# Kernel optimization log

Measured on AMD Instinct MI355X. Metric: run time of the kernel, lower is better.

Reference implementation:

```python
import jax, jax.numpy as jnp
import numpy as np

NUM_EMBEDDINGS = 1024
EMBEDDING_DIM = 256


def setup_inputs() -> dict:
    key = jax.random.key(0)
    k1, k2 = jax.random.split(key)
    z_e = jax.random.normal(k1, (32, EMBEDDING_DIM, 32, 32), dtype=jnp.float32)
    codebook = jax.random.normal(k2, (NUM_EMBEDDINGS, EMBEDDING_DIM), dtype=jnp.float32)
    return {"z_e": z_e, "codebook": codebook}


def reference(z_e, codebook):
    # z_e: [B, C, H, W] with C == embedding_dim; codebook: [K, C]
    B, C, H, W = z_e.shape
    K = codebook.shape[0]
    # _flatten: NCHW -> NHWC -> [N, C]
    z_nhwc = jnp.transpose(z_e, (0, 2, 3, 1))
    z_flat = z_nhwc.reshape(-1, C)
    # _compute_distances: ||z||^2 + ||e||^2 - 2 z e^T  -> [N, K]
    z_sq = jnp.sum(z_flat * z_flat, axis=1, keepdims=True)
    e_sq = jnp.sum(codebook * codebook, axis=1)
    distances = z_sq + e_sq - 2.0 * jnp.matmul(z_flat, codebook.T)
    # argmin + one-hot scatter (_build_encodings)
    indices = jnp.argmin(distances, axis=1)
    encodings = jax.nn.one_hot(indices, K, dtype=z_flat.dtype)  # [N, K]
    # _compute_perplexity
    avg_probs = jnp.mean(encodings, axis=0)
    perplexity = jnp.exp(-jnp.sum(avg_probs * jnp.log(avg_probs + 1e-10)))
    return distances, indices, encodings, perplexity
```

## Files before the change

### kernel.cpp

```cpp
#include <hip/hip_runtime.h>
#include <math.h>

#define N_ROWS 32768
#define K_CODES 1024
#define C_DIM 256
#define HW 1024

#define OFF_DIST 0
#define OFF_IDX  (N_ROWS * K_CODES)
#define OFF_ENC  (OFF_IDX + N_ROWS)
#define OFF_PERP (OFF_ENC + N_ROWS * K_CODES)

typedef __attribute__((ext_vector_type(8))) short short8;
typedef __attribute__((ext_vector_type(4))) float f32x4;

__device__ inline unsigned short bf16_rn(float x) {
    unsigned int u = __float_as_uint(x);
    unsigned int r = u + 0x7FFFu + ((u >> 16) & 1u);
    return (unsigned short)(r >> 16);
}
__device__ inline float bf16_to_f(unsigned short h) {
    return __uint_as_float(((unsigned int)h) << 16);
}

__device__ __forceinline__ void gl2lds16(const unsigned short* g, char* l) {
    __builtin_amdgcn_global_load_lds(
        (const __attribute__((address_space(1))) unsigned int*)g,
        (__attribute__((address_space(3))) unsigned int*)l, 16, 0, 0);
}

__global__ __launch_bounds__(256) void prep_kernel(
        const float* __restrict__ z, const float* __restrict__ cb,
        unsigned short* __restrict__ z_hi, unsigned short* __restrict__ z_lo,
        unsigned short* __restrict__ cb_hi, unsigned short* __restrict__ cb_lo,
        float* __restrict__ zsq, float* __restrict__ esq) {
    const int bid = blockIdx.x;
    const int t = threadIdx.x;

    if (bid >= 256) {
        const int lane = t & 63;
        const int k = (bid - 256) * 4 + (t >> 6);
        float4 v = *reinterpret_cast<const float4*>(cb + (size_t)k * C_DIM + lane * 4);
        float s = v.x * v.x + v.y * v.y + v.z * v.z + v.w * v.w;
        ushort4 h, l;
        h.x = bf16_rn(v.x); l.x = bf16_rn(v.x - bf16_to_f(h.x));
        h.y = bf16_rn(v.y); l.y = bf16_rn(v.y - bf16_to_f(h.y));
        h.z = bf16_rn(v.z); l.z = bf16_rn(v.z - bf16_to_f(h.z));
        h.w = bf16_rn(v.w); l.w = bf16_rn(v.w - bf16_to_f(h.w));
        *reinterpret_cast<ushort4*>(cb_hi + (size_t)k * C_DIM + lane * 4) = h;
        *reinterpret_cast<ushort4*>(cb_lo + (size_t)k * C_DIM + lane * 4) = l;
#pragma unroll
        for (int m = 1; m < 64; m <<= 1) s += __shfl_xor(s, m);
        if (lane == 0) esq[k] = s;
        return;
    }

    __shared__ float st[64][132];
    const int b = bid >> 3;
    const int hw0 = (bid & 7) * 128;

    const int c_r  = t >> 5;
    const int hw_r = (t & 31) * 4;
    const int hw_w = t >> 1;
    const int ch   = (t & 1) * 32;
    const int n    = b * HW + hw0 + hw_w;

    float zacc = 0.f;

    for (int c0 = 0; c0 < C_DIM; c0 += 64) {
#pragma unroll
        for (int it = 0; it < 8; ++it) {
            int c_l = it * 8 + c_r;
            float4 v = *reinterpret_cast<const float4*>(
                z + (size_t)b * (C_DIM * HW) + (size_t)(c0 + c_l) * HW + hw0 + hw_r);
            *reinterpret_cast<float4*>(&st[c_l][hw_r]) = v;
        }
        __syncthreads();

        short8 hv[4], lv[4];
#pragma unroll
        for (int j = 0; j < 32; ++j) {
            float x = st[ch + j][hw_w];
            unsigned short h = bf16_rn(x);
            unsigned short lo = bf16_rn(x - bf16_to_f(h));
            hv[j >> 3][j & 7] = (short)h;
            lv[j >> 3][j & 7] = (short)lo;
            zacc = fmaf(x, x, zacc);
        }
        unsigned short* hp = z_hi + (size_t)n * C_DIM + c0 + ch;
        unsigned short* lp = z_lo + (size_t)n * C_DIM + c0 + ch;
#pragma unroll
        for (int q = 0; q < 4; ++q) {
            *reinterpret_cast<short8*>(hp + q * 8) = hv[q];
            *reinterpret_cast<short8*>(lp + q * 8) = lv[q];
        }
        __syncthreads();
    }
    float o = __shfl_xor(zacc, 1);
    if ((t & 1) == 0) zsq[n] = zacc + o;
}

#define KSTEPS 24

__global__ __launch_bounds__(512) void dist_mfma_kernel(
        const unsigned short* __restrict__ z_hi,
        const unsigned short* __restrict__ z_lo,
        const unsigned short* __restrict__ cb_hi,
        const unsigned short* __restrict__ cb_lo,
        const float* __restrict__ zsq, const float* __restrict__ esq,
        float* __restrict__ dist, float2* __restrict__ partial) {
    __shared__ __align__(16) unsigned short As[2][128 * 32];
    __shared__ __align__(16) unsigned short Bs[2][256 * 32];
    __shared__ float2 pb[128][4];

    const int t = threadIdx.x;
    const int lane = t & 63, wid = t >> 6;
    const int wy = wid >> 2, wx = wid & 3;
    const int l15 = lane & 15, l4 = lane >> 4;

    const int swz = (blockIdx.x & 7) * 128 + (blockIdx.x >> 3);
    const int kbi = swz & 3;
    const int kb = kbi * 256;
    const int nb = (swz >> 2) * 128;

#define STAGE(buf_, s_) do {                                                   \
        const int sp_ = (s_) >> 3;                                             \
        const int sc0_ = ((s_) & 7) * 32;                                      \
        const unsigned short* Ap_ = (sp_ == 2) ? z_lo : z_hi;                  \
        const unsigned short* Bp_ = (sp_ == 1) ? cb_lo : cb_hi;                \
        const int wb_ = (t & ~63) * 16;                                        \
        gl2lds16(Ap_ + (size_t)(nb + (t >> 2)) * C_DIM + sc0_ + (t & 3) * 8,   \
                 (char*)(&As[buf_][0]) + wb_);                                 \
        gl2lds16(Bp_ + (size_t)(kb + (t >> 2)) * C_DIM + sc0_ + (t & 3) * 8,   \
                 (char*)(&Bs[buf_][0]) + wb_);                                 \
        gl2lds16(Bp_ + (size_t)(kb + 128 + (t >> 2)) * C_DIM + sc0_ + (t & 3) * 8, \
                 (char*)(&Bs[buf_][0]) + 8192 + wb_);                          \
    } while (0)

    f32x4 acc[4][4] = {};

    STAGE(0, 0);
    __syncthreads();

    for (int s = 0; s < KSTEPS; ++s) {
        const int cur = s & 1;
        if (s < KSTEPS - 1) STAGE(cur ^ 1, s + 1);

        short8 av[4], bv[4];
#pragma unroll
        for (int mi = 0; mi < 4; ++mi)
            av[mi] = *reinterpret_cast<const short8*>(
                &As[cur][(wy * 64 + mi * 16 + l15) * 32 + l4 * 8]);
#pragma unroll
        for (int ci = 0; ci < 4; ++ci)
            bv[ci] = *reinterpret_cast<const short8*>(
                &Bs[cur][(wx * 64 + ci * 16 + l15) * 32 + l4 * 8]);

#pragma unroll
        for (int mi = 0; mi < 4; ++mi)
#pragma unroll
            for (int ci = 0; ci < 4; ++ci)
                acc[mi][ci] = __builtin_amdgcn_mfma_f32_16x16x32_bf16(
                    av[mi], bv[ci], acc[mi][ci], 0, 0, 0);
        __syncthreads();
    }
#undef STAGE

    float zsv[4][4];
#pragma unroll
    for (int mi = 0; mi < 4; ++mi)
#pragma unroll
        for (int r = 0; r < 4; ++r)
            zsv[mi][r] = zsq[nb + wy * 64 + mi * 16 + l4 * 4 + r];
    float esv[4];
#pragma unroll
    for (int ci = 0; ci < 4; ++ci)
        esv[ci] = esq[kb + wx * 64 + ci * 16 + l15];

    float best[4][4];
    int bidx[4][4];
#pragma unroll
    for (int mi = 0; mi < 4; ++mi)
#pragma unroll
        for (int r = 0; r < 4; ++r) { best[mi][r] = 1e30f; bidx[mi][r] = K_CODES; }

#pragma unroll
    for (int mi = 0; mi < 4; ++mi) {
#pragma unroll
        for (int r = 0; r < 4; ++r) {
            int row = nb + wy * 64 + mi * 16 + l4 * 4 + r;
            float* drow = dist + (size_t)row * K_CODES;
#pragma unroll
            for (int ci = 0; ci < 4; ++ci) {
                int col = kb + wx * 64 + ci * 16 + l15;
                float d = zsv[mi][r] + esv[ci] - 2.f * acc[mi][ci][r];
                drow[col] = d;
                if (d < best[mi][r]) { best[mi][r] = d; bidx[mi][r] = col; }
            }
        }
    }

#pragma unroll
    for (int m = 1; m < 16; m <<= 1) {
#pragma unroll
        for (int mi = 0; mi < 4; ++mi)
#pragma unroll
            for (int r = 0; r < 4; ++r) {
                float ob = __shfl_xor(best[mi][r], m);
                int   oi = __shfl_xor(bidx[mi][r], m);
                if (ob < best[mi][r] || (ob == best[mi][r] && oi < bidx[mi][r])) {
                    best[mi][r] = ob; bidx[mi][r] = oi;
                }
            }
    }

    if (l15 == 0) {
#pragma unroll
        for (int mi = 0; mi < 4; ++mi)
#pragma unroll
            for (int r = 0; r < 4; ++r) {
                int rl = wy * 64 + mi * 16 + l4 * 4 + r;
                pb[rl][wx] = make_float2(best[mi][r], (float)bidx[mi][r]);
            }
    }
    __syncthreads();
    if (t < 128) {
        float2 bv2 = pb[t][0];
#pragma unroll
        for (int w = 1; w < 4; ++w) {
            float2 c = pb[t][w];
            if (c.x < bv2.x) bv2 = c;
        }
        partial[(size_t)kbi * N_ROWS + nb + t] = bv2;
    }
}

__global__ __launch_bounds__(256) void combenc_kernel(
        const float2* __restrict__ partial, float* __restrict__ idx_out,
        int* __restrict__ idx_int, float* __restrict__ enc) {
    __shared__ int sidx[16];
    const int t = threadIdx.x;
    const int r0 = blockIdx.x * 16;
    if (t < 16) {
        int n = r0 + t;
        float2 bv = partial[n];
#pragma unroll
        for (int kb = 1; kb < 4; ++kb) {
            float2 c = partial[(size_t)kb * N_ROWS + n];
            if (c.x < bv.x) bv = c;
        }
        idx_out[n] = bv.y;
        idx_int[n] = (int)bv.y;
        sidx[t] = (int)bv.y;
    }
    __syncthreads();
    const int k0 = t * 4;
#pragma unroll 4
    for (int r = 0; r < 16; ++r) {
        int bi = sidx[r];
        float4 v;
        v.x = (k0 + 0 == bi) ? 1.0f : 0.0f;
        v.y = (k0 + 1 == bi) ? 1.0f : 0.0f;
        v.z = (k0 + 2 == bi) ? 1.0f : 0.0f;
        v.w = (k0 + 3 == bi) ? 1.0f : 0.0f;
        *reinterpret_cast<float4*>(enc + (size_t)(r0 + r) * K_CODES + k0) = v;
    }
}

__global__ __launch_bounds__(1024) void perp_kernel(const int* __restrict__ idxi,
                                                    float* __restrict__ out) {
    __shared__ int hist[K_CODES];
    __shared__ float wsum[16];
    const int t = threadIdx.x;
    hist[t] = 0;
    __syncthreads();
    for (int n = t; n < N_ROWS; n += 1024)
        atomicAdd(&hist[idxi[n]], 1);
    __syncthreads();
    float p = (float)hist[t] * (1.0f / (float)N_ROWS);
    float s = p * logf(p + 1e-10f);
#pragma unroll
    for (int off = 32; off > 0; off >>= 1) s += __shfl_down(s, off);
    if ((t & 63) == 0) wsum[t >> 6] = s;
    __syncthreads();
    if (t == 0) {
        float tot = 0.f;
#pragma unroll
        for (int w = 0; w < 16; ++w) tot += wsum[w];
        out[0] = expf(-tot);
    }
}

extern "C" void kernel_launch(void* const* d_in, const int* in_sizes, int n_in,
                              void* d_out, int out_size, void* d_ws, size_t ws_size,
                              hipStream_t stream) {
    const float* z  = (const float*)d_in[0];
    const float* cb = (const float*)d_in[1];
    float* out  = (float*)d_out;
    float* dist = out + OFF_DIST;
    float* idxo = out + OFF_IDX;
    float* enc  = out + OFF_ENC;
    float* perp = out + OFF_PERP;

    char* wsb = (char*)d_ws;
    float*  zsq  = (float*)(wsb + 0);
    float*  esq  = (float*)(wsb + 131072);
    int*    idxi = (int*)(wsb + 135168);
    float2* part = (float2*)(wsb + 266240);

    unsigned short* z_hi  = (unsigned short*)enc;
    unsigned short* z_lo  = z_hi + (size_t)N_ROWS * C_DIM;
    unsigned short* cb_hi = z_lo + (size_t)N_ROWS * C_DIM;
    unsigned short* cb_lo = cb_hi + (size_t)K_CODES * C_DIM;

    prep_kernel<<<512, 256, 0, stream>>>(z, cb, z_hi, z_lo, cb_hi, cb_lo, zsq, esq);
    dist_mfma_kernel<<<1024, 512, 0, stream>>>(z_hi, z_lo, cb_hi, cb_lo,
                                               zsq, esq, dist, part);
    combenc_kernel<<<N_ROWS / 16, 256, 0, stream>>>(part, idxo, idxi, enc);
    perp_kernel<<<1, 1024, 0, stream>>>(idxi, perp);
}
```

Baseline: 390.1 us.

## Triple-buffer LDS staging with swizzled layout and single barrier per step

Moves the MFMA distance kernel from double to triple buffering. Loads are issued two steps ahead and gated with explicit vmcnt waits, so each K-step needs one barrier instead of two. It also XOR-swizzles the 16-byte chunks within each LDS row to cut bank conflicts on the fragment reads, and adds a min-blocks-per-CU hint of 4 to launch_bounds. The larger LDS footprint may reduce occupancy, and the hand-written waitcnt assumes exactly three outstanding loads per stage.

```diff
diff --git a/kernel.cpp b/kernel.cpp
--- a/kernel.cpp
+++ b/kernel.cpp
@@ -102,15 +102,15 @@
 
 #define KSTEPS 24
 
-__global__ __launch_bounds__(512) void dist_mfma_kernel(
+__global__ __launch_bounds__(512, 4) void dist_mfma_kernel(
         const unsigned short* __restrict__ z_hi,
         const unsigned short* __restrict__ z_lo,
         const unsigned short* __restrict__ cb_hi,
         const unsigned short* __restrict__ cb_lo,
         const float* __restrict__ zsq, const float* __restrict__ esq,
         float* __restrict__ dist, float2* __restrict__ partial) {
-    __shared__ __align__(16) unsigned short As[2][128 * 32];
-    __shared__ __align__(16) unsigned short Bs[2][256 * 32];
+    __shared__ __align__(16) unsigned short As[3][128 * 32];
+    __shared__ __align__(16) unsigned short Bs[3][256 * 32];
     __shared__ float2 pb[128][4];
 
     const int t = threadIdx.x;
@@ -122,39 +122,57 @@
     const int kbi = swz & 3;
     const int kb = kbi * 256;
     const int nb = (swz >> 2) * 128;
+
+    const int srow = t >> 2;
+    const int soct = ((t & 3) ^ ((t >> 3) & 3)) * 8;
+    const int wb   = (t & ~63) * 16;
+
+    const int swzo = (l4 ^ ((l15 >> 1) & 3)) * 16;
 
 #define STAGE(buf_, s_) do {                                                   \
         const int sp_ = (s_) >> 3;                                             \
         const int sc0_ = ((s_) & 7) * 32;                                      \
         const unsigned short* Ap_ = (sp_ == 2) ? z_lo : z_hi;                  \
         const unsigned short* Bp_ = (sp_ == 1) ? cb_lo : cb_hi;                \
-        const int wb_ = (t & ~63) * 16;                                        \
-        gl2lds16(Ap_ + (size_t)(nb + (t >> 2)) * C_DIM + sc0_ + (t & 3) * 8,   \
-                 (char*)(&As[buf_][0]) + wb_);                                 \
-        gl2lds16(Bp_ + (size_t)(kb + (t >> 2)) * C_DIM + sc0_ + (t & 3) * 8,   \
-                 (char*)(&Bs[buf_][0]) + wb_);                                 \
-        gl2lds16(Bp_ + (size_t)(kb + 128 + (t >> 2)) * C_DIM + sc0_ + (t & 3) * 8, \
-                 (char*)(&Bs[buf_][0]) + 8192 + wb_);                          \
+        char* ab_ = (char*)(&As[buf_][0]) + wb;                                \
+        char* bb_ = (char*)(&Bs[buf_][0]) + wb;                                \
+        gl2lds16(Ap_ + (size_t)(nb + srow) * C_DIM + sc0_ + soct, ab_);        \
+        gl2lds16(Bp_ + (size_t)(kb + srow) * C_DIM + sc0_ + soct, bb_);        \
+        gl2lds16(Bp_ + (size_t)(kb + 128 + srow) * C_DIM + sc0_ + soct,        \
+                 bb_ + 8192);                                                  \
     } while (0)
 
     f32x4 acc[4][4] = {};
 
     STAGE(0, 0);
-    __syncthreads();
-
+    STAGE(1, 1);
+
+#pragma unroll
     for (int s = 0; s < KSTEPS; ++s) {
-        const int cur = s & 1;
-        if (s < KSTEPS - 1) STAGE(cur ^ 1, s + 1);
+        if (s < KSTEPS - 1) {
+            asm volatile("s_waitcnt vmcnt(3)" ::: "memory");
+        } else {
+            asm volatile("s_waitcnt vmcnt(0)" ::: "memory");
+        }
+        __builtin_amdgcn_sched_barrier(0);
+        __builtin_amdgcn_s_barrier();
+        __builtin_amdgcn_sched_barrier(0);
+
+        const int buf = s % 3;
+        const char* Ab = (const char*)(&As[buf][0]);
+        const char* Bb = (const char*)(&Bs[buf][0]);
 
         short8 av[4], bv[4];
 #pragma unroll
         for (int mi = 0; mi < 4; ++mi)
             av[mi] = *reinterpret_cast<const short8*>(
-                &As[cur][(wy * 64 + mi * 16 + l15) * 32 + l4 * 8]);
+                Ab + (wy * 64 + mi * 16 + l15) * 64 + swzo);
 #pragma unroll
         for (int ci = 0; ci < 4; ++ci)
             bv[ci] = *reinterpret_cast<const short8*>(
-                &Bs[cur][(wx * 64 + ci * 16 + l15) * 32 + l4 * 8]);
+                Bb + (wx * 64 + ci * 16 + l15) * 64 + swzo);
+
+        if (s < KSTEPS - 2) STAGE((s + 2) % 3, s + 2);
 
 #pragma unroll
         for (int mi = 0; mi < 4; ++mi)
@@ -162,7 +180,6 @@
             for (int ci = 0; ci < 4; ++ci)
                 acc[mi][ci] = __builtin_amdgcn_mfma_f32_16x16x32_bf16(
                     av[mi], bv[ci], acc[mi][ci], 0, 0, 0);
-        __syncthreads();
     }
 #undef STAGE
 
```

Result: slower. 402.4 us (+3.1%).
